# Performance work log

Measured on AMD Instinct MI355X. Metric: run time of the kernel, lower is better.

## Reference

```python
import jax, jax.numpy as jnp
import numpy as np

B, S, H, NH = 2, 2048, 768, 12
HD = H // NH
MEM_W = 0.5  # memory_weight
LN_EPS = 1e-5


def setup_inputs() -> dict:
    key = jax.random.key(0)
    ks = jax.random.split(key, 12)
    xav = lambda k: jax.random.uniform(k, (H, H), jnp.float32, -1.0, 1.0) * np.sqrt(6.0 / (H + H))
    return {
        "hidden_states": jax.random.normal(ks[0], (B, S, H), jnp.float32),
        "cross_states": jax.random.normal(ks[1], (B, S, H), jnp.float32),
        "attention_mask": jnp.ones((B, 1, S, S), jnp.int32),
        "memory_tensors": jax.random.normal(ks[2], (2, B, S, H), jnp.float32),
        "dynamic_factor": jax.random.uniform(ks[3], (B, S, 1), jnp.float32),
        "Wq": xav(ks[4]), "bq": jnp.zeros((H,), jnp.float32),
        "Wk": xav(ks[5]), "bk": jnp.zeros((H,), jnp.float32),
        "Wv": xav(ks[6]), "bv": jnp.zeros((H,), jnp.float32),
        "Wo": xav(ks[7]), "bo": jnp.zeros((H,), jnp.float32),
        "gate": jnp.ones((1,), jnp.float32),
        "gate_bias": jnp.zeros((1,), jnp.float32),
        "ln_g": jnp.ones((H,), jnp.float32),
        "ln_b": jnp.zeros((H,), jnp.float32),
    }


def _layernorm(x, g, b):
    mu = jnp.mean(x, axis=-1, keepdims=True)
    var = jnp.mean(jnp.square(x - mu), axis=-1, keepdims=True)
    return (x - mu) * jax.lax.rsqrt(var + LN_EPS) * g + b


def reference(hidden_states, cross_states, attention_mask, memory_tensors,
              dynamic_factor, Wq, bq, Wk, bk, Wv, bv, Wo, bo,
              gate, gate_bias, ln_g, ln_b):
    x = _layernorm(hidden_states, ln_g, ln_b)
    q = x @ Wq + bq                      # [B,S,H]
    k = cross_states @ Wk + bk
    v = cross_states @ Wv + bv
    k = k + memory_tensors[0] * MEM_W    # memory injection into K/V
    v = v + memory_tensors[1] * MEM_W

    q = q.reshape(B, S, NH, HD).transpose(0, 2, 1, 3)  # [B,NH,S,HD]
    k = k.reshape(B, S, NH, HD).transpose(0, 2, 1, 3)
    v = v.reshape(B, S, NH, HD).transpose(0, 2, 1, 3)

    scores = jnp.einsum("bhqd,bhkd->bhqk", q, k) / np.sqrt(HD)
    scores = jnp.where(attention_mask == 0, -jnp.inf, scores)
    attn = jax.nn.softmax(scores, axis=-1)
    out = jnp.einsum("bhqk,bhkd->bhqd", attn, v)       # [B,NH,S,HD]
    out = out.transpose(0, 2, 1, 3).reshape(B, S, H)

    out = out @ Wo + bo
    out = out * gate + gate_bias
    out = out * dynamic_factor
    return out
```

## Files before the change

### kernel.cpp

```cpp
#include <hip/hip_runtime.h>
#include <hip/hip_bf16.h>
#include <stdint.h>

#define BB   2
#define SS   2048
#define HH   768
#define NHH  12
#define HDD  64
#define BSS  (BB*SS)
#define NBH  (BB*NHH)
#define ROWS_BH (NBH*SS)
#define NSPLIT 2

typedef unsigned short u16;
typedef unsigned int   u32;
typedef __attribute__((ext_vector_type(8))) short bf16x8_t;
typedef __attribute__((ext_vector_type(4))) float f32x4;
typedef __attribute__((ext_vector_type(16))) float f32x16;
typedef __attribute__((ext_vector_type(2))) u32   u32x2;
typedef __attribute__((ext_vector_type(4))) u32   u32x4;

#define MFMA16(a, b, c) __builtin_amdgcn_mfma_f32_16x16x32_bf16((a), (b), (c), 0, 0, 0)
#define MFMA32(a, b, c) __builtin_amdgcn_mfma_f32_32x32x16_bf16((a), (b), (c), 0, 0, 0)

__device__ __forceinline__ float b2f(u16 u) {
    u32 x = ((u32)u) << 16; float f; __builtin_memcpy(&f, &x, 4); return f;
}
__device__ __forceinline__ u16 f2b(float f) {
    u32 x; __builtin_memcpy(&x, &f, 4);
    u32 r = x + 0x7fffu + ((x >> 16) & 1u);
    return (u16)(r >> 16);
}
__device__ __forceinline__ u32 cvtpk(float a, float b) {
    u32 r;
    __asm__("v_cvt_pk_bf16_f32 %0, %1, %2" : "=v"(r) : "v"(a), "v"(b));
    return r;
}
__device__ __forceinline__ void async16(const u16* g, u16* l) {
    __builtin_amdgcn_global_load_lds(
        (const __attribute__((address_space(1))) void*)g,
        (__attribute__((address_space(3))) void*)l, 16, 0, 0);
}

__global__ __launch_bounds__(256) void prep_kernel(
    const float* __restrict__ Wq, const float* __restrict__ Wk,
    const float* __restrict__ Wv, const float* __restrict__ Wo,
    u16* __restrict__ Wt,
    const float* __restrict__ hid, const float* __restrict__ cross,
    const float* __restrict__ g, const float* __restrict__ bb,
    u16* __restrict__ xln, u16* __restrict__ crossb,
    const int* __restrict__ mask, u32* __restrict__ bits,
    u32* __restrict__ wrow)
{
    int id = blockIdx.x;
    int t = threadIdx.x;

    if (id < 576) {
        int mat = id / 144, rem = id % 144;
        int by = rem / 12, bx = rem % 12;
        const float* src = (mat == 0) ? Wq : (mat == 1) ? Wk : (mat == 2) ? Wv : Wo;
        u16* dst = Wt + (size_t)mat * 768 * 768;

        __shared__ float sm[64][68];
        int r0 = by * 64, c0 = bx * 64;
        #pragma unroll
        for (int it = 0; it < 4; ++it) {
            int c = t + it * 256;
            int r = c >> 4, sg = c & 15;
            *(float4*)&sm[r][sg * 4] = *(const float4*)&src[(size_t)(r0 + r) * 768 + c0 + sg * 4];
        }
        __syncthreads();
        #pragma unroll
        for (int it = 0; it < 2; ++it) {
            int c = t + it * 256;
            int rr = c >> 3, sg = c & 7;
            u16 tmp[8] __attribute__((aligned(16)));
            #pragma unroll
            for (int j = 0; j < 8; ++j) tmp[j] = f2b(sm[sg * 8 + j][rr]);
            *(u32x4*)&dst[(size_t)(c0 + rr) * 768 + r0 + sg * 8] = *(u32x4*)tmp;
        }
        return;
    }

    if (id < 2624) {
        int lid = id - 576;
        int y = lid >> 10, bx = lid & 1023;
        int wv = t >> 6, lane = t & 63;
        int row = bx * 4 + wv;

        if (y == 1) {
            const float* xr = cross + (size_t)row * 768;
            u16* o = crossb + (size_t)row * 768;
            #pragma unroll
            for (int c = 0; c < 3; ++c) {
                float4 f = *(const float4*)&xr[c * 256 + lane * 4];
                u16 t4[4] __attribute__((aligned(8)));
                t4[0] = f2b(f.x); t4[1] = f2b(f.y); t4[2] = f2b(f.z); t4[3] = f2b(f.w);
                *(u32x2*)&o[c * 256 + lane * 4] = *(u32x2*)t4;
            }
            return;
        }

        const float* xr = hid + (size_t)row * 768;
        float v[12];
        float s = 0.f, s2 = 0.f;
        #pragma unroll
        for (int c = 0; c < 3; ++c) {
            float4 f = *(const float4*)&xr[c * 256 + lane * 4];
            v[c*4+0] = f.x; v[c*4+1] = f.y; v[c*4+2] = f.z; v[c*4+3] = f.w;
            s  += f.x + f.y + f.z + f.w;
            s2 += f.x*f.x + f.y*f.y + f.z*f.z + f.w*f.w;
        }
        #pragma unroll
        for (int off = 1; off < 64; off <<= 1) {
            s  += __shfl_xor(s,  off, 64);
            s2 += __shfl_xor(s2, off, 64);
        }
        float mu  = s  * (1.f / 768.f);
        float var = s2 * (1.f / 768.f) - mu * mu;
        float rs  = 1.f / sqrtf(var + 1e-5f);
        #pragma unroll
        for (int c = 0; c < 3; ++c) {
            float4 gg = *(const float4*)&g [c * 256 + lane * 4];
            float4 bv = *(const float4*)&bb[c * 256 + lane * 4];
            u16 o[4] __attribute__((aligned(8)));
            o[0] = f2b((v[c*4+0] - mu) * rs * gg.x + bv.x);
            o[1] = f2b((v[c*4+1] - mu) * rs * gg.y + bv.y);
            o[2] = f2b((v[c*4+2] - mu) * rs * gg.z + bv.z);
            o[3] = f2b((v[c*4+3] - mu) * rs * gg.w + bv.w);
            *(u32x2*)&xln[(size_t)row * 768 + c * 256 + lane * 4] = *(u32x2*)o;
        }
        return;
    }

    {
        int mid = id - 2624;
        int w = mid * 256 + t;
        const int4* p = (const int4*)(mask + (size_t)w * 32);
        u32 v = 0;
        #pragma unroll
        for (int i = 0; i < 8; ++i) {
            int4 m = p[i];
            v |= ((m.x != 0) ? 1u : 0u) << (4 * i + 0);
            v |= ((m.y != 0) ? 1u : 0u) << (4 * i + 1);
            v |= ((m.z != 0) ? 1u : 0u) << (4 * i + 2);
            v |= ((m.w != 0) ? 1u : 0u) << (4 * i + 3);
        }
        bits[w] = v;
        unsigned long long ball = __ballot(v == 0xffffffffu);
        if ((t & 63) == 0) {
            u32 wr = 0;
            #pragma unroll
            for (int kt = 0; kt < 32; ++kt)
                if (((ball >> (2 * kt)) & 3ull) == 3ull) wr |= (1u << kt);
            wrow[w >> 6] = wr;
        }
    }
}

__device__ __forceinline__ void gemm6464_main(const u16* __restrict__ A,
                                              const u16* __restrict__ W,
                                              int m0, int n0,
                                              f32x4 acc[2][2])
{
    __shared__ __attribute__((aligned(16))) u16 AsL[64 * 64];
    __shared__ __attribute__((aligned(16))) u16 BsL[64 * 64];
    int t = threadIdx.x;
    int wv = t >> 6, lane = t & 63, lm = lane & 15, quad = lane >> 4;
    int wr = wv >> 1, wc = wv & 1;

    for (int kt = 0; kt < 768 / 64; ++kt) {
        __syncthreads();
        #pragma unroll
        for (int it = 0; it < 2; ++it) {
            int c = t + it * 256;
            int row = c >> 3, cs = (c & 7) ^ (row & 7);
            async16(A + (size_t)(m0 + row) * 768 + kt * 64 + cs * 8, &AsL[c * 8]);
        }
        #pragma unroll
        for (int it = 0; it < 2; ++it) {
            int c = t + it * 256;
            int row = c >> 3, cs = (c & 7) ^ (row & 7);
            async16(W + (size_t)(n0 + row) * 768 + kt * 64 + cs * 8, &BsL[c * 8]);
        }
        __syncthreads();
        #pragma unroll
        for (int kk = 0; kk < 2; ++kk) {
            bf16x8_t af[2], bfv[2];
            #pragma unroll
            for (int i = 0; i < 2; ++i) {
                int r = wr * 32 + i * 16 + lm;
                af[i] = *(const bf16x8_t*)&AsL[(r * 8 + ((kk * 4 + quad) ^ (r & 7))) * 8];
            }
            #pragma unroll
            for (int j = 0; j < 2; ++j) {
                int r = wc * 32 + j * 16 + lm;
                bfv[j] = *(const bf16x8_t*)&BsL[(r * 8 + ((kk * 4 + quad) ^ (r & 7))) * 8];
            }
            #pragma unroll
            for (int i = 0; i < 2; ++i)
                #pragma unroll
                for (int j = 0; j < 2; ++j)
                    acc[i][j] = MFMA16(af[i], bfv[j], acc[i][j]);
        }
    }
}

__global__ __launch_bounds__(256) void qkv_gemm(
    const u16* __restrict__ xln, const u16* __restrict__ crossb,
    const u16* __restrict__ Wt,  const float* __restrict__ bq,
    const float* __restrict__ bk, const float* __restrict__ bv,
    const float* __restrict__ mem,
    u16* __restrict__ Qb, u16* __restrict__ Kb, u16* __restrict__ VtG)
{
    int z = blockIdx.z;
    const u16* A      = (z == 0) ? xln : crossb;
    const u16* W      = Wt + (size_t)z * 768 * 768;
    const float* bias = (z == 0) ? bq : (z == 1) ? bk : bv;
    const float* mp   = (z == 0) ? (const float*)nullptr : mem + (size_t)(z - 1) * BSS * HH;

    f32x4 z4 = {0.f, 0.f, 0.f, 0.f};
    f32x4 acc[2][2];
    #pragma unroll
    for (int i = 0; i < 2; ++i)
        #pragma unroll
        for (int j = 0; j < 2; ++j) acc[i][j] = z4;

    int m0 = blockIdx.x * 64, n0 = blockIdx.y * 64;
    gemm6464_main(A, W, m0, n0, acc);

    int t = threadIdx.x, wv = t >> 6, lane = t & 63, lm = lane & 15, quad = lane >> 4;
    int wr = wv >> 1, wc = wv & 1;
    int row0 = m0 + wr * 32 + quad * 4;
    int col0 = n0 + wc * 32 + lm;

    if (z == 2) {
        #pragma unroll
        for (int j = 0; j < 2; ++j) {
            int cg = col0 + j * 16;
            float bz = bias[cg];
            int h = cg >> 6, d = cg & 63;
            #pragma unroll
            for (int i = 0; i < 2; ++i) {
                int rg = row0 + i * 16;
                int b = rg >> 11, s = rg & 2047;
                u16 ob[4] __attribute__((aligned(8)));
                #pragma unroll
                for (int e = 0; e < 4; ++e) {
                    float v = acc[i][j][e] + bz + 0.5f * mp[(size_t)(rg + e) * HH + cg];
                    ob[e] = f2b(v);
                }
                *(u32x2*)&VtG[((size_t)(b * NHH + h) * 64 + d) * SS + s] = *(u32x2*)ob;
            }
        }
        return;
    }

    u16* out = (z == 0) ? Qb : Kb;
    #pragma unroll
    for (int j = 0; j < 2; ++j) {
        int cg = col0 + j * 16;
        float bz = bias[cg];
        #pragma unroll
        for (int i = 0; i < 2; ++i) {
            int rg = row0 + i * 16;
            #pragma unroll
            for (int e = 0; e < 4; ++e) {
                float v = acc[i][j][e] + bz;
                if (mp) v += 0.5f * mp[(size_t)(rg + e) * HH + cg];
                out[(size_t)(rg + e) * HH + cg] = f2b(v);
            }
        }
    }
}

__global__ __launch_bounds__(256, 3) void attn_kernel(
    const u16* __restrict__ Q, const u16* __restrict__ K,
    const u16* __restrict__ VtG, const u32* __restrict__ mbits,
    const u32* __restrict__ wrow,
    u16* __restrict__ Pacc, float* __restrict__ Pl, int ksteps)
{
    __shared__ __attribute__((aligned(16))) u16 KsL[2][64 * 64];
    __shared__ __attribute__((aligned(16))) u16 VtL[2][64 * 64];

    int x  = blockIdx.x;
    int qt = blockIdx.y;
    int bh = x >> 1;
    int z  = x & 1;
    int b = bh / NHH, h = bh % NHH;
    int t = threadIdx.x;
    int wv = t >> 6, lane = t & 63;
    int q31 = lane & 31, hi = lane >> 5;

    int qbase = qt * 128 + wv * 32;
    const u16* qp = Q + (size_t)(b * SS + qbase + q31) * HH + h * 64 + hi * 8;
    bf16x8_t qf0 = *(const bf16x8_t*)&qp[0];
    bf16x8_t qf1 = *(const bf16x8_t*)&qp[16];
    bf16x8_t qf2 = *(const bf16x8_t*)&qp[32];
    bf16x8_t qf3 = *(const bf16x8_t*)&qp[48];

    f32x16 acc0 = {};
    f32x16 acc1 = {};
    float l_lane = 0.f;

    const float SC = 0.18033688011112042f;

    u32 wl = wrow[b * SS + qbase + q31];
    const u32* mrow = &mbits[(size_t)(b * SS + qbase + q31) * (SS / 32)];

    const u16* Kb0 = K + (size_t)(b * SS) * HH + h * 64;
    const u16* Vb0 = VtG + (size_t)bh * 64 * SS;

    auto STAGE = [&](int pp, int kt) {
        int k0 = kt * 64;
        #pragma unroll
        for (int it = 0; it < 2; ++it) {
            int c = t + it * 256;
            int rr = c >> 3, ss = (c & 7) ^ (rr & 7);
            async16(Kb0 + (size_t)(k0 + rr) * HH + ss * 8, &KsL[pp][c * 8]);
            async16(Vb0 + (size_t)rr * SS + k0 + ss * 8,   &VtL[pp][c * 8]);
        }
    };

    int kt0 = z * ksteps, ktE = kt0 + ksteps;
    STAGE(0, kt0);
    __syncthreads();

    for (int kt = kt0; kt < ktE; ++kt) {
        int p = (kt - kt0) & 1;
        if (kt + 1 < ktE) STAGE(p ^ 1, kt + 1);

        bool ok = __all((int)((wl >> kt) & 1u));
        unsigned long long mw = ~0ull;
        if (!ok) {
            u32x2 u = *(const u32x2*)&mrow[kt * 2];
            mw = ((unsigned long long)u.y << 32) | (unsigned long long)u.x;
        }

        #pragma unroll
        for (int kb = 0; kb < 2; ++kb) {
            f32x16 sc = {};
            #pragma unroll
            for (int step = 0; step < 4; ++step) {
                int row = kb * 32 + q31;
                int ch = (step * 2 + hi) ^ (row & 7);
                bf16x8_t kf = *(const bf16x8_t*)&KsL[p][(row * 8 + ch) * 8];
                bf16x8_t qf = (step == 0) ? qf0 : (step == 1) ? qf1 : (step == 2) ? qf2 : qf3;
                sc = MFMA32(kf, qf, sc);
            }

            #pragma unroll
            for (int r = 0; r < 16; ++r) {
                float pv = __builtin_amdgcn_exp2f(sc[r] * SC);
                if (!ok) {
                    int kbit = kb * 32 + (r & 3) + 8 * (r >> 2) + 4 * hi;
                    if (!((mw >> kbit) & 1ull)) pv = 0.f;
                }
                sc[r] = pv;
                l_lane += pv;
            }

            #pragma unroll
            for (int s2 = 0; s2 < 2; ++s2) {
                u32 P0 = cvtpk(sc[8 * s2 + 0], sc[8 * s2 + 1]);
                u32 P1 = cvtpk(sc[8 * s2 + 2], sc[8 * s2 + 3]);
                u32 P2 = cvtpk(sc[8 * s2 + 4], sc[8 * s2 + 5]);
                u32 P3 = cvtpk(sc[8 * s2 + 6], sc[8 * s2 + 7]);
                auto s02 = __builtin_amdgcn_permlane32_swap((int)P0, (int)P2, false, false);
                auto s13 = __builtin_amdgcn_permlane32_swap((int)P1, (int)P3, false, false);
                u32x4 w;
                w.x = (u32)s02[0]; w.y = (u32)s13[0];
                w.z = (u32)s02[1]; w.w = (u32)s13[1];
                bf16x8_t pf = __builtin_bit_cast(bf16x8_t, w);

                int vrow0 = q31;
                int vrow1 = 32 + q31;
                int ch = kb * 4 + s2 * 2 + hi;
                bf16x8_t vf0 = *(const bf16x8_t*)&VtL[p][(vrow0 * 8 + (ch ^ (vrow0 & 7))) * 8];
                bf16x8_t vf1 = *(const bf16x8_t*)&VtL[p][(vrow1 * 8 + (ch ^ (vrow1 & 7))) * 8];
                acc0 = MFMA32(pf, vf0, acc0);
                acc1 = MFMA32(pf, vf1, acc1);
            }
        }

        __syncthreads();
    }

    l_lane += __shfl_xor(l_lane, 32, 64);

    size_t prow0 = ((size_t)z * NBH + bh) * SS + qt * 128 + wv * 32;
    #pragma unroll
    for (int r = 0; r < 16; ++r) {
        int qrow = (r & 3) + 8 * (r >> 2) + 4 * hi;
        Pacc[(prow0 + qrow) * 64 + q31]      = f2b(acc0[r]);
        Pacc[(prow0 + qrow) * 64 + 32 + q31] = f2b(acc1[r]);
    }
    if (lane < 32) Pl[prow0 + lane] = l_lane;
}

__global__ __launch_bounds__(256) void attn_merge(
    const u16* __restrict__ Pacc, const float* __restrict__ Pl,
    u16* __restrict__ AO)
{
    int t = threadIdx.x;
    int r = blockIdx.x * 64 + (t >> 2);
    int dseg = (t & 3) * 16;

    float lsum = Pl[r] + Pl[(size_t)ROWS_BH + r];

    float o[16];
    #pragma unroll
    for (int i = 0; i < 16; ++i) o[i] = 0.f;
    #pragma unroll
    for (int s = 0; s < NSPLIT; ++s) {
        const u16* ap = &Pacc[((size_t)s * ROWS_BH + r) * 64 + dseg];
        u32x4 a0 = *(const u32x4*)ap;
        u32x4 a1 = *(const u32x4*)(ap + 8);
        u32 wa[8];
        wa[0]=a0.x; wa[1]=a0.y; wa[2]=a0.z; wa[3]=a0.w;
        wa[4]=a1.x; wa[5]=a1.y; wa[6]=a1.z; wa[7]=a1.w;
        #pragma unroll
        for (int i = 0; i < 8; ++i) {
            o[2*i]   += b2f((u16)(wa[i] & 0xffff));
            o[2*i+1] += b2f((u16)(wa[i] >> 16));
        }
    }
    float inv = 1.f / lsum;
    int bh = r >> 11, q = r & 2047;
    int b = bh / NHH, h = bh % NHH;
    u16 ob[16] __attribute__((aligned(16)));
    #pragma unroll
    for (int i = 0; i < 16; ++i) ob[i] = f2b(o[i] * inv);
    u16* op = &AO[((size_t)(b * SS + q)) * HH + h * 64 + dseg];
    *(u32x4*)op       = *(u32x4*)ob;
    *(u32x4*)(op + 8) = *(u32x4*)(ob + 8);
}

__global__ __launch_bounds__(256) void out_gemm(
    const u16* __restrict__ AO, const u16* __restrict__ Wt,
    const float* __restrict__ bo, const float* __restrict__ gate,
    const float* __restrict__ gbias, const float* __restrict__ dyn,
    float* __restrict__ out)
{
    __shared__ __attribute__((aligned(16))) u16 AsL[32 * 64];
    __shared__ __attribute__((aligned(16))) u16 BsL[64 * 64];

    f32x4 z4 = {0.f, 0.f, 0.f, 0.f};
    f32x4 acc[2];
    acc[0] = z4; acc[1] = z4;

    int m0 = blockIdx.x * 32, n0 = blockIdx.y * 64;
    int t = threadIdx.x;
    int wv = t >> 6, lane = t & 63, lm = lane & 15, quad = lane >> 4;
    int wr = wv >> 1, wc = wv & 1;

    for (int kt = 0; kt < 768 / 64; ++kt) {
        __syncthreads();
        {
            int c = t;
            int row = c >> 3, cs = (c & 7) ^ (row & 7);
            async16(AO + (size_t)(m0 + row) * 768 + kt * 64 + cs * 8, &AsL[c * 8]);
        }
        #pragma unroll
        for (int it = 0; it < 2; ++it) {
            int c = t + it * 256;
            int row = c >> 3, cs = (c & 7) ^ (row & 7);
            async16(Wt + (size_t)(n0 + row) * 768 + kt * 64 + cs * 8, &BsL[c * 8]);
        }
        __syncthreads();
        #pragma unroll
        for (int kk = 0; kk < 2; ++kk) {
            bf16x8_t af, bfv[2];
            {
                int r = wr * 16 + lm;
                af = *(const bf16x8_t*)&AsL[(r * 8 + ((kk * 4 + quad) ^ (r & 7))) * 8];
            }
            #pragma unroll
            for (int j = 0; j < 2; ++j) {
                int r = wc * 32 + j * 16 + lm;
                bfv[j] = *(const bf16x8_t*)&BsL[(r * 8 + ((kk * 4 + quad) ^ (r & 7))) * 8];
            }
            #pragma unroll
            for (int j = 0; j < 2; ++j)
                acc[j] = MFMA16(af, bfv[j], acc[j]);
        }
    }

    float gv = gate[0];
    float gb = gbias[0];
    int row0 = m0 + wr * 16 + quad * 4;
    int col0 = n0 + wc * 32 + lm;
    #pragma unroll
    for (int j = 0; j < 2; ++j) {
        int cg = col0 + j * 16;
        float bz = bo[cg];
        #pragma unroll
        for (int e = 0; e < 4; ++e) {
            int rg = row0 + e;
            float v = acc[j][e] + bz;
            v = v * gv + gb;
            v *= dyn[rg];
            out[(size_t)rg * HH + cg] = v;
        }
    }
}

extern "C" void kernel_launch(void* const* d_in, const int* in_sizes, int n_in,
                              void* d_out, int out_size, void* d_ws, size_t ws_size,
                              hipStream_t stream)
{
    (void)in_sizes; (void)n_in; (void)out_size; (void)ws_size;

    const float* hid   = (const float*)d_in[0];
    const float* cross = (const float*)d_in[1];
    const int*   amask = (const int*)d_in[2];
    const float* mem   = (const float*)d_in[3];
    const float* dyn   = (const float*)d_in[4];
    const float* Wq    = (const float*)d_in[5];
    const float* bq    = (const float*)d_in[6];
    const float* Wk    = (const float*)d_in[7];
    const float* bk    = (const float*)d_in[8];
    const float* Wv    = (const float*)d_in[9];
    const float* bv    = (const float*)d_in[10];
    const float* Wo    = (const float*)d_in[11];
    const float* bo    = (const float*)d_in[12];
    const float* gate  = (const float*)d_in[13];
    const float* gbias = (const float*)d_in[14];
    const float* lng   = (const float*)d_in[15];
    const float* lnb   = (const float*)d_in[16];

    char* p = (char*)d_ws;
    u16* Wt   = (u16*)p; p += (size_t)4 * 768 * 768 * 2;
    u32* mb   = (u32*)p; p += (size_t)BB * SS * (SS / 32) * 4;
    u32* wrow = (u32*)p; p += (size_t)BSS * 4;
    u16* xln  = (u16*)p; p += (size_t)BSS * HH * 2;
    u16* crb  = (u16*)p; p += (size_t)BSS * HH * 2;
    u16* Qb   = (u16*)p; p += (size_t)BSS * HH * 2;
    u16* Kb   = (u16*)p; p += (size_t)BSS * HH * 2;
    u16* VtG  = (u16*)p; p += (size_t)BSS * HH * 2;
    u16* Pacc  = xln;
    float* Pl  = (float*)Wt;
    u16* AO    = Kb;

    prep_kernel <<<dim3(3648),           256, 0, stream>>>(
        Wq, Wk, Wv, Wo, Wt, hid, cross, lng, lnb, xln, crb, amask, mb, wrow);
    qkv_gemm    <<<dim3(64, 12, 3),      256, 0, stream>>>(
        xln, crb, Wt, bq, bk, bv, mem, Qb, Kb, VtG);
    attn_kernel <<<dim3(48, 16),         256, 0, stream>>>(
        Qb, Kb, VtG, mb, wrow, Pacc, Pl, SS / 64 / NSPLIT);
    attn_merge  <<<dim3(ROWS_BH / 64),   256, 0, stream>>>(Pacc, Pl, AO);
    out_gemm    <<<dim3(128, 12),        256, 0, stream>>>(
        AO, Wt + (size_t)3 * 768 * 768, bo, gate, gbias, dyn, (float*)d_out);
}
```

Baseline: 243.4 us.

## Fuse split-K attention merge into attention kernel via last-block atomic counter

Removes the separate attn_merge kernel. Each attention block now increments a per-(head, query-tile) counter after writing its partial results, and the second block to finish reads both partials, normalizes them and writes the attention output directly. Merged output is written into the Q buffer, which is safe because only the two blocks of that tile read that Q region. This saves a kernel launch and lets the merge overlap with other attention blocks, at the cost of an extra memset, an atomic per block and some imbalance where the last blocks do extra work.

```diff
diff --git a/kernel.cpp b/kernel.cpp
--- a/kernel.cpp
+++ b/kernel.cpp
@@ -278,7 +278,8 @@
     const u16* __restrict__ Q, const u16* __restrict__ K,
     const u16* __restrict__ VtG, const u32* __restrict__ mbits,
     const u32* __restrict__ wrow,
-    u16* __restrict__ Pacc, float* __restrict__ Pl, int ksteps)
+    u16* __restrict__ Pacc, float* __restrict__ Pl,
+    u32* __restrict__ flags, u16* __restrict__ AO, int ksteps)
 {
     __shared__ __attribute__((aligned(16))) u16 KsL[2][64 * 64];
     __shared__ __attribute__((aligned(16))) u16 VtL[2][64 * 64];
@@ -396,44 +397,45 @@
         Pacc[(prow0 + qrow) * 64 + 32 + q31] = f2b(acc1[r]);
     }
     if (lane < 32) Pl[prow0 + lane] = l_lane;
-}
-
-__global__ __launch_bounds__(256) void attn_merge(
-    const u16* __restrict__ Pacc, const float* __restrict__ Pl,
-    u16* __restrict__ AO)
-{
-    int t = threadIdx.x;
-    int r = blockIdx.x * 64 + (t >> 2);
-    int dseg = (t & 3) * 16;
-
-    float lsum = Pl[r] + Pl[(size_t)ROWS_BH + r];
-
-    float o[16];
+
+    __syncthreads();
+    __shared__ u32 sWin;
+    if (t == 0) {
+        __threadfence();
+        u32 old = atomicAdd(&flags[bh * 16 + qt], 1u);
+        sWin = (old == 1u) ? 1u : 0u;
+    }
+    __syncthreads();
+    if (sWin == 0) return;
+    __threadfence();
+
+    int rl4 = t >> 2, dseg = (t & 3) * 16;
     #pragma unroll
-    for (int i = 0; i < 16; ++i) o[i] = 0.f;
-    #pragma unroll
-    for (int s = 0; s < NSPLIT; ++s) {
-        const u16* ap = &Pacc[((size_t)s * ROWS_BH + r) * 64 + dseg];
-        u32x4 a0 = *(const u32x4*)ap;
-        u32x4 a1 = *(const u32x4*)(ap + 8);
-        u32 wa[8];
-        wa[0]=a0.x; wa[1]=a0.y; wa[2]=a0.z; wa[3]=a0.w;
-        wa[4]=a1.x; wa[5]=a1.y; wa[6]=a1.z; wa[7]=a1.w;
+    for (int half = 0; half < 2; ++half) {
+        int rl = rl4 + half * 64;
+        size_t rbase = (size_t)bh * SS + qt * 128 + rl;
+        float lsum = Pl[rbase] + Pl[(size_t)ROWS_BH + rbase];
+        float inv = 1.f / lsum;
+        const u16* a0p = &Pacc[rbase * 64 + dseg];
+        const u16* a1p = &Pacc[((size_t)ROWS_BH + rbase) * 64 + dseg];
+        u32x4 a0 = *(const u32x4*)a0p;
+        u32x4 a1 = *(const u32x4*)(a0p + 8);
+        u32x4 c0 = *(const u32x4*)a1p;
+        u32x4 c1 = *(const u32x4*)(a1p + 8);
+        u32 w0[8] = {a0.x, a0.y, a0.z, a0.w, a1.x, a1.y, a1.z, a1.w};
+        u32 w1[8] = {c0.x, c0.y, c0.z, c0.w, c1.x, c1.y, c1.z, c1.w};
+        u16 ob[16] __attribute__((aligned(16)));
         #pragma unroll
         for (int i = 0; i < 8; ++i) {
-            o[2*i]   += b2f((u16)(wa[i] & 0xffff));
-            o[2*i+1] += b2f((u16)(wa[i] >> 16));
-        }
-    }
-    float inv = 1.f / lsum;
-    int bh = r >> 11, q = r & 2047;
-    int b = bh / NHH, h = bh % NHH;
-    u16 ob[16] __attribute__((aligned(16)));
-    #pragma unroll
-    for (int i = 0; i < 16; ++i) ob[i] = f2b(o[i] * inv);
-    u16* op = &AO[((size_t)(b * SS + q)) * HH + h * 64 + dseg];
-    *(u32x4*)op       = *(u32x4*)ob;
-    *(u32x4*)(op + 8) = *(u32x4*)(ob + 8);
+            float lo  = (b2f((u16)(w0[i] & 0xffff)) + b2f((u16)(w1[i] & 0xffff))) * inv;
+            float hh2 = (b2f((u16)(w0[i] >> 16))    + b2f((u16)(w1[i] >> 16)))    * inv;
+            ob[2 * i]     = f2b(lo);
+            ob[2 * i + 1] = f2b(hh2);
+        }
+        u16* op = &AO[((size_t)(b * SS + qt * 128 + rl)) * HH + h * 64 + dseg];
+        *(u32x4*)op       = *(u32x4*)ob;
+        *(u32x4*)(op + 8) = *(u32x4*)(ob + 8);
+    }
 }
 
 __global__ __launch_bounds__(256) void out_gemm(
@@ -540,15 +542,16 @@
     u16* VtG  = (u16*)p; p += (size_t)BSS * HH * 2;
     u16* Pacc  = xln;
     float* Pl  = (float*)Wt;
-    u16* AO    = Kb;
+    u32* flags = (u32*)((char*)Wt + 448 * 1024);
+    u16* AO    = Qb;
 
     prep_kernel <<<dim3(3648),           256, 0, stream>>>(
         Wq, Wk, Wv, Wo, Wt, hid, cross, lng, lnb, xln, crb, amask, mb, wrow);
     qkv_gemm    <<<dim3(64, 12, 3),      256, 0, stream>>>(
         xln, crb, Wt, bq, bk, bv, mem, Qb, Kb, VtG);
+    hipMemsetAsync(flags, 0, NBH * 16 * sizeof(u32), stream);
     attn_kernel <<<dim3(48, 16),         256, 0, stream>>>(
-        Qb, Kb, VtG, mb, wrow, Pacc, Pl, SS / 64 / NSPLIT);
-    attn_merge  <<<dim3(ROWS_BH / 64),   256, 0, stream>>>(Pacc, Pl, AO);
+        Qb, Kb, VtG, mb, wrow, Pacc, Pl, flags, AO, SS / 64 / NSPLIT);
     out_gemm    <<<dim3(128, 12),        256, 0, stream>>>(
         AO, Wt + (size_t)3 * 768 * 768, bo, gate, gbias, dyn, (float*)d_out);
 }
```

Measured after the change: 352.3 us. 44.7% more time.
